# Kernel optimization log

Measured on AMD Instinct MI355X. Metric: run time of the kernel, lower is better.

## Reference

```python
import math
import jax, jax.numpy as jnp
import numpy as np

B, H, W, CV = 8, 64, 64, 256
T, CT = 77, 512
NH, TOP_M = 8, 5
CLAMP = 2.0

def _ln(x, g, b, eps=1e-5):
    mu = x.mean(-1, keepdims=True)
    var = ((x - mu) ** 2).mean(-1, keepdims=True)
    return (x - mu) / jnp.sqrt(var + eps) * g + b

def _l2norm(x, eps=1e-6):
    n = jnp.sqrt((x * x).sum(-1, keepdims=True))
    return x / jnp.maximum(n, eps)

def _xavier(key, fan_in, fan_out):
    a = math.sqrt(6.0 / (fan_in + fan_out))
    return jax.random.uniform(key, (fan_in, fan_out), jnp.float32, -a, a)

def setup_inputs() -> dict:
    key = jax.random.key(0)
    ks = jax.random.split(key, 12)
    inp = {
        'visual_features': jax.random.normal(ks[0], (B, H, W, CV), jnp.float32),
        'text_features': jax.random.normal(ks[1], (B, T, CT), jnp.float32),
        'Wq': _xavier(ks[2], CV, CV), 'bq': jnp.zeros((CV,), jnp.float32),
        'Wk': _xavier(ks[3], CT, CV), 'bk': jnp.zeros((CV,), jnp.float32),
        'Wv': _xavier(ks[4], CT, CV), 'bv': jnp.zeros((CV,), jnp.float32),
        'Wo': _xavier(ks[5], CV, CV), 'bo': jnp.zeros((CV,), jnp.float32),
        'g1': jnp.ones((CV,), jnp.float32), 'b1': jnp.zeros((CV,), jnp.float32),
        'g2': jnp.ones((CV,), jnp.float32), 'b2': jnp.zeros((CV,), jnp.float32),
        'W_ffn1': jax.random.normal(ks[6], (CV, 4 * CV), jnp.float32) * 0.02,
        'b_ffn1': jnp.zeros((4 * CV,), jnp.float32),
        'W_ffn2': jax.random.normal(ks[7], (4 * CV, CV), jnp.float32) * 0.02,
        'b_ffn2': jnp.zeros((CV,), jnp.float32),
        'logit_scale': jnp.float32(math.log(1.0 / 0.07)),
        'alpha': jnp.float32(0.1),
    }
    return inp

def _topm_mask(sim, m):
    # keep only top-m entries along last axis (scatter of top-k indices)
    t = sim.shape[-1]
    _, topi = jax.lax.top_k(sim, m)
    keep = jax.vmap(lambda idx: jnp.zeros((t,), bool).at[idx].set(True))(
        topi.reshape(-1, m)).reshape(sim.shape)
    return jnp.where(keep, sim, -jnp.inf)

def _forward(visual_features, text_features, Wq, bq, Wk, bk, Wv, bv, Wo, bo,
             g1, b1, g2, b2, W_ffn1, b_ffn1, W_ffn2, b_ffn2, logit_scale, alpha):
    b, h, w, cv = visual_features.shape
    n = h * w
    dh = cv // NH
    x = _ln(visual_features, g1, b1).reshape(b, n, cv)      # Pre-LN, (B,N,Cv)
    q = (x @ Wq + bq).reshape(b, n, NH, dh)
    k = (text_features @ Wk + bk).reshape(b, T, NH, dh)
    v = (text_features @ Wv + bv).reshape(b, T, NH, dh)
    q = _l2norm(q); k = _l2norm(k)                           # cosine attention
    scale = jnp.exp(jnp.clip(logit_scale, -CLAMP, CLAMP)) / jnp.sqrt(jnp.float32(dh))
    sim = jnp.einsum('bnhd,bthd->bnht', q, k) * scale        # (B,N,H,T)
    pad = jnp.abs(text_features).sum(-1) <= 1e-6             # (B,T) pad tokens
    sim = jnp.where(pad[:, None, None, :], -jnp.inf, sim)
    sim = _topm_mask(sim, TOP_M)
    attn = jax.nn.softmax(sim, axis=-1)
    all_pad = pad.all(axis=1)                                # (B,)
    attn = jnp.where(all_pad[:, None, None, None], 0.0, attn)
    aligned = jnp.einsum('bnht,bthd->bnhd', attn, v).reshape(b, n, cv)
    aligned = aligned @ Wo + bo
    y = x + alpha * aligned
    y = _ln(y, g2, b2)
    hdn = jax.nn.gelu(y @ W_ffn1 + b_ffn1, approximate=False)
    y = y + (hdn @ W_ffn2 + b_ffn2)
    return y.reshape(b, h, w, cv)

def reference(visual_features, text_features, Wq, bq, Wk, bk, Wv, bv, Wo, bo,
              g1, b1, g2, b2, W_ffn1, b_ffn1, W_ffn2, b_ffn2, logit_scale, alpha):
    return _forward(visual_features, text_features, Wq, bq, Wk, bk, Wv, bv, Wo, bo,
                    g1, b1, g2, b2, W_ffn1, b_ffn1, W_ffn2, b_ffn2, logit_scale, alpha)
```

## Files before the change

### kernel.cpp

```cpp
#include <hip/hip_runtime.h>
#include <math.h>

#define NB   8
#define NPIX 4096
#define MROW 32768
#define CV_  256
#define TT   77
#define CT_  512
#define NH_  8
#define DH_  32
#define BT_  616

typedef __bf16 bf16x8 __attribute__((ext_vector_type(8)));
typedef float  f32x4  __attribute__((ext_vector_type(4)));

__device__ __forceinline__ float bf2f(unsigned short u) {
  return __uint_as_float(((unsigned)u) << 16);
}
__device__ __forceinline__ unsigned short f2b(float f) {
  unsigned u = __float_as_uint(f);
  return (unsigned short)((u + 0x7FFFu + ((u >> 16) & 1u)) >> 16);
}
__device__ __forceinline__ unsigned pack2(float lo, float hi) {
  return ((unsigned)f2b(hi) << 16) | (unsigned)f2b(lo);
}
__device__ __forceinline__ void async_copy16(const unsigned short* g,
                                             unsigned short* l) {
  __builtin_amdgcn_global_load_lds(
      (const __attribute__((address_space(1))) void*)g,
      (__attribute__((address_space(3))) void*)l, 16, 0, 0);
}
__device__ __forceinline__ float gelu_t(float v) {
  float p = v * fmaf(0.0713548162726f, v * v, 1.59576912161f);
  float e = __expf(p);
  return v - v / (e + 1.0f);
}

__global__ __launch_bounds__(256) void prep_kernel(
    const float* __restrict__ visual, const float* __restrict__ g1,
    const float* __restrict__ b1, unsigned short* __restrict__ xbuf,
    const float* __restrict__ s0, const float* __restrict__ s1,
    const float* __restrict__ s2, const float* __restrict__ s3,
    const float* __restrict__ s4, const float* __restrict__ s5,
    unsigned short* __restrict__ d0, unsigned short* __restrict__ d1,
    unsigned short* __restrict__ d2, unsigned short* __restrict__ d3,
    unsigned short* __restrict__ d4, unsigned short* __restrict__ d5,
    const float* __restrict__ bk, const float* __restrict__ bv,
    float* __restrict__ bkv, const float* __restrict__ text,
    float* __restrict__ padb) {
  __shared__ unsigned short tl[64 * 68];
  int bx = blockIdx.x;
  int tid = threadIdx.x;
  int wave = tid >> 6, lane = tid & 63;
  if (bx < 8192) {
    int row = bx * 4 + wave;
    size_t base = (size_t)row * 256 + lane * 4;
    float4 f = *reinterpret_cast<const float4*>(visual + base);
    float v0 = f.x, v1 = f.y, v2 = f.z, v3 = f.w;
    float s = v0 + v1 + v2 + v3;
    float q = v0 * v0 + v1 * v1 + v2 * v2 + v3 * v3;
#pragma unroll
    for (int off = 1; off < 64; off <<= 1) {
      s += __shfl_xor(s, off);
      q += __shfl_xor(q, off);
    }
    float mean = s * (1.0f / 256.0f);
    float var  = q * (1.0f / 256.0f) - mean * mean;
    float rstd = rsqrtf(var + 1e-5f);
    float4 gv = *reinterpret_cast<const float4*>(g1 + lane * 4);
    float4 bv4 = *reinterpret_cast<const float4*>(b1 + lane * 4);
    ushort4 o;
    o.x = f2b((v0 - mean) * rstd * gv.x + bv4.x);
    o.y = f2b((v1 - mean) * rstd * gv.y + bv4.y);
    o.z = f2b((v2 - mean) * rstd * gv.z + bv4.z);
    o.w = f2b((v3 - mean) * rstd * gv.w + bv4.w);
    *reinterpret_cast<ushort4*>(xbuf + base) = o;
    return;
  }
  if (bx < 8416) {
    int ti = bx - 8192;
    const float* src; unsigned short* dst; int R, C, m;
    if      (ti < 16)  { src = s0; dst = d0; R = 256;  C = 256;  m = ti; }
    else if (ti < 48)  { src = s1; dst = d1; R = 512;  C = 256;  m = ti - 16; }
    else if (ti < 80)  { src = s2; dst = d2; R = 512;  C = 256;  m = ti - 48; }
    else if (ti < 96)  { src = s3; dst = d3; R = 256;  C = 256;  m = ti - 80; }
    else if (ti < 160) { src = s4; dst = d4; R = 256;  C = 1024; m = ti - 96; }
    else               { src = s5; dst = d5; R = 1024; C = 256;  m = ti - 160; }
    int tpc = C >> 6;
    int tr = m / tpc, tc = m % tpc;
#pragma unroll
    for (int i = 0; i < 4; ++i) {
      int lin = tid + i * 256;
      int r = lin >> 4, c4 = (lin & 15) * 4;
      float4 f = *reinterpret_cast<const float4*>(
          src + (size_t)(tr * 64 + r) * C + tc * 64 + c4);
      tl[(c4 + 0) * 68 + r] = f2b(f.x);
      tl[(c4 + 1) * 68 + r] = f2b(f.y);
      tl[(c4 + 2) * 68 + r] = f2b(f.z);
      tl[(c4 + 3) * 68 + r] = f2b(f.w);
    }
    __syncthreads();
#pragma unroll
    for (int i = 0; i < 4; ++i) {
      int lin = tid + i * 256;
      int c = lin >> 4, r4 = (lin & 15) * 4;
      ushort4 u = *reinterpret_cast<const ushort4*>(&tl[c * 68 + r4]);
      *reinterpret_cast<ushort4*>(
          dst + (size_t)(tc * 64 + c) * R + tr * 64 + r4) = u;
    }
    return;
  }
  if (bx == 8416) {
    bkv[tid] = bk[tid];
    bkv[256 + tid] = bv[tid];
    return;
  }
  {
    int row = (bx - 8417) * 4 + wave;
    const float* tr = text + (size_t)row * CT_ + lane * 8;
    float4 f0 = *reinterpret_cast<const float4*>(tr);
    float4 f1 = *reinterpret_cast<const float4*>(tr + 4);
    float s = fabsf(f0.x) + fabsf(f0.y) + fabsf(f0.z) + fabsf(f0.w)
            + fabsf(f1.x) + fabsf(f1.y) + fabsf(f1.z) + fabsf(f1.w);
#pragma unroll
    for (int off = 1; off < 64; off <<= 1) s += __shfl_xor(s, off);
    if (lane == 0) padb[row] = (s <= 1e-6f) ? 1.0f : 0.0f;
  }
}

__global__ __launch_bounds__(256) void qkv_kernel(
    const unsigned short* __restrict__ xb, const unsigned short* __restrict__ WqT,
    const float* __restrict__ bq, unsigned short* __restrict__ qout,
    const float* __restrict__ text, const unsigned short* __restrict__ WkvT,
    const float* __restrict__ bkv, float* __restrict__ kout,
    float* __restrict__ vout) {
  __shared__ unsigned short lA[4096];
  __shared__ unsigned short lB[4096];
  int tid = threadIdx.x;
  int lane = tid & 63, wave = tid >> 6;
  int l15 = lane & 15, quad = lane >> 4;
  if (blockIdx.x < 1024) {
    int bm = (blockIdx.x >> 2) * 128, bn = (blockIdx.x & 3) * 64;
    int wm = (wave & 1) * 64, wn = (wave >> 1) * 32;
    int crow = lane >> 2, ccol = (lane & 3) * 8;
    f32x4 acc[4][2] = {};
    for (int k0 = 0; k0 < 256; k0 += 32) {
#pragma unroll
      for (int ch = 0; ch < 2; ++ch) {
        int c = wave * 2 + ch;
        async_copy16(xb + (size_t)(bm + c * 16 + crow) * 256 + k0 + ccol,
                     &lA[c * 512]);
      }
      async_copy16(WqT + (size_t)(bn + wave * 16 + crow) * 256 + k0 + ccol,
                   &lB[wave * 512]);
      __syncthreads();
      bf16x8 af[4], bfr[2];
#pragma unroll
      for (int mi = 0; mi < 4; ++mi)
        af[mi] = *reinterpret_cast<const bf16x8*>(&lA[(wm + mi * 16 + l15) * 32 + quad * 8]);
#pragma unroll
      for (int ni = 0; ni < 2; ++ni)
        bfr[ni] = *reinterpret_cast<const bf16x8*>(&lB[(wn + ni * 16 + l15) * 32 + quad * 8]);
#pragma unroll
      for (int mi = 0; mi < 4; ++mi)
#pragma unroll
        for (int ni = 0; ni < 2; ++ni)
          acc[mi][ni] = __builtin_amdgcn_mfma_f32_16x16x32_bf16(af[mi], bfr[ni],
                                                                acc[mi][ni], 0, 0, 0);
      __syncthreads();
    }
#pragma unroll
    for (int mi = 0; mi < 4; ++mi) {
#pragma unroll
      for (int ni = 0; ni < 2; ++ni) {
        int gcol = bn + wn + ni * 16 + l15;
        float bsf = bq[gcol];
#pragma unroll
        for (int r = 0; r < 4; ++r) {
          int grow = bm + wm + mi * 16 + quad * 4 + r;
          qout[(size_t)grow * 256 + gcol] = f2b(acc[mi][ni][r] + bsf);
        }
      }
    }
  } else {
    int i = blockIdx.x - 1024;
    int bm = (i % 10) * 64, bn = (i / 10) * 64;
    int srow = tid >> 2, sc8 = (tid & 3) * 8;
    int wm = (wave & 1) * 32, wn = (wave >> 1) * 32;
    f32x4 acc[2][2] = {};
    int gm = bm + srow, gn = bn + srow;
    const bool aok = (gm < BT_);
    for (int k0 = 0; k0 < CT_; k0 += 32) {
      uint4 apk = make_uint4(0, 0, 0, 0);
      if (aok) {
        const float* Af = text + (size_t)gm * CT_ + k0 + sc8;
        float4 f0 = *reinterpret_cast<const float4*>(Af);
        float4 f1 = *reinterpret_cast<const float4*>(Af + 4);
        apk.x = pack2(f0.x, f0.y); apk.y = pack2(f0.z, f0.w);
        apk.z = pack2(f1.x, f1.y); apk.w = pack2(f1.z, f1.w);
      }
      uint4 bpk = *reinterpret_cast<const uint4*>(WkvT + (size_t)gn * CT_ + k0 + sc8);
      *reinterpret_cast<uint4*>(&lA[srow * 40 + sc8]) = apk;
      *reinterpret_cast<uint4*>(&lB[srow * 40 + sc8]) = bpk;
      __syncthreads();
      bf16x8 a0 = *reinterpret_cast<const bf16x8*>(&lA[(wm + l15) * 40 + quad * 8]);
      bf16x8 a1 = *reinterpret_cast<const bf16x8*>(&lA[(wm + 16 + l15) * 40 + quad * 8]);
      bf16x8 b0 = *reinterpret_cast<const bf16x8*>(&lB[(wn + l15) * 40 + quad * 8]);
      bf16x8 b1 = *reinterpret_cast<const bf16x8*>(&lB[(wn + 16 + l15) * 40 + quad * 8]);
      acc[0][0] = __builtin_amdgcn_mfma_f32_16x16x32_bf16(a0, b0, acc[0][0], 0, 0, 0);
      acc[0][1] = __builtin_amdgcn_mfma_f32_16x16x32_bf16(a0, b1, acc[0][1], 0, 0, 0);
      acc[1][0] = __builtin_amdgcn_mfma_f32_16x16x32_bf16(a1, b0, acc[1][0], 0, 0, 0);
      acc[1][1] = __builtin_amdgcn_mfma_f32_16x16x32_bf16(a1, b1, acc[1][1], 0, 0, 0);
      __syncthreads();
    }
#pragma unroll
    for (int mt = 0; mt < 2; ++mt) {
#pragma unroll
      for (int nt = 0; nt < 2; ++nt) {
        int gcol = bn + wn + nt * 16 + l15;
        float bsf = bkv[gcol];
#pragma unroll
        for (int r = 0; r < 4; ++r) {
          int grow = bm + wm + mt * 16 + quad * 4 + r;
          if (grow >= BT_) continue;
          float v = acc[mt][nt][r] + bsf;
          if (gcol < 256) kout[(size_t)grow * 256 + gcol] = v;
          else            vout[(size_t)grow * 256 + gcol - 256] = v;
        }
      }
    }
  }
}

__global__ __launch_bounds__(256) void gemm_oln(
    const unsigned short* __restrict__ A, const unsigned short* __restrict__ Bt,
    const float* __restrict__ bias, const unsigned short* __restrict__ xres,
    const float* __restrict__ alpha_ptr,
    const float* __restrict__ g2, const float* __restrict__ b2,
    unsigned short* __restrict__ ybf, float* __restrict__ yf32) {
  __shared__ unsigned short sm[9216];
  unsigned short* lA = sm;
  unsigned short* lB = sm + 1024;
  unsigned short* yt = sm;
  const int K = 256;
  int tid = threadIdx.x;
  int bm = blockIdx.x * 32;
  int lane = tid & 63, wave = tid >> 6;
  int wm = (wave & 1) * 16, wn = (wave >> 1) * 128;
  int l15 = lane & 15, quad = lane >> 4;
  int crow = lane >> 2, ccol = (lane & 3) * 8;
  f32x4 acc[8] = {};
  for (int k0 = 0; k0 < K; k0 += 32) {
    if (wave < 2)
      async_copy16(A + (size_t)(bm + wave * 16 + crow) * K + k0 + ccol,
                   &lA[wave * 512]);
#pragma unroll
    for (int ch = wave; ch < 16; ch += 4)
      async_copy16(Bt + (size_t)(ch * 16 + crow) * K + k0 + ccol,
                   &lB[ch * 512]);
    __syncthreads();
    bf16x8 af, bfr[8];
    af = *reinterpret_cast<const bf16x8*>(&lA[(wm + l15) * 32 + quad * 8]);
#pragma unroll
    for (int ni = 0; ni < 8; ++ni)
      bfr[ni] = *reinterpret_cast<const bf16x8*>(&lB[(wn + ni * 16 + l15) * 32 + quad * 8]);
#pragma unroll
    for (int ni = 0; ni < 8; ++ni)
      acc[ni] = __builtin_amdgcn_mfma_f32_16x16x32_bf16(af, bfr[ni],
                                                        acc[ni], 0, 0, 0);
    __syncthreads();
  }
  float alpha = *alpha_ptr;
#pragma unroll
  for (int ni = 0; ni < 8; ++ni) {
    int gcol = wn + ni * 16 + l15;
    float bsf = bias[gcol];
#pragma unroll
    for (int r = 0; r < 4; ++r) {
      int lrow = wm + quad * 4 + r;
      float v = acc[ni][r] + bsf;
      float y0 = bf2f(xres[(size_t)(bm + lrow) * 256 + gcol]) + alpha * v;
      yt[lrow * 256 + gcol] = f2b(y0);
    }
  }
  __syncthreads();
  for (int it = 0; it < 8; ++it) {
    int row = wave * 8 + it;
    ushort4 u = *reinterpret_cast<const ushort4*>(&yt[row * 256 + lane * 4]);
    float v0 = bf2f(u.x), v1 = bf2f(u.y), v2 = bf2f(u.z), v3 = bf2f(u.w);
    float s = v0 + v1 + v2 + v3;
    float q = v0 * v0 + v1 * v1 + v2 * v2 + v3 * v3;
#pragma unroll
    for (int off = 1; off < 64; off <<= 1) {
      s += __shfl_xor(s, off);
      q += __shfl_xor(q, off);
    }
    float mean = s * (1.0f / 256.0f);
    float var  = q * (1.0f / 256.0f) - mean * mean;
    float rstd = rsqrtf(var + 1e-5f);
    float4 gv = *reinterpret_cast<const float4*>(g2 + lane * 4);
    float4 bv = *reinterpret_cast<const float4*>(b2 + lane * 4);
    float o0 = (v0 - mean) * rstd * gv.x + bv.x;
    float o1 = (v1 - mean) * rstd * gv.y + bv.y;
    float o2 = (v2 - mean) * rstd * gv.z + bv.z;
    float o3 = (v3 - mean) * rstd * gv.w + bv.w;
    size_t base = (size_t)(bm + row) * 256 + lane * 4;
    ushort4 ob;
    ob.x = f2b(o0); ob.y = f2b(o1); ob.z = f2b(o2); ob.w = f2b(o3);
    *reinterpret_cast<ushort4*>(ybf + base) = ob;
    *reinterpret_cast<float4*>(yf32 + base) = make_float4(o0, o1, o2, o3);
  }
}

#define SSTR 83
#define VSTR 33
#define NEGBIG -3.0e38f
__device__ __forceinline__ void ins5(float sv, float& tv0, float& tv1,
                                     float& tv2, float& tv3, float& tv4) {
  bool g0 = sv > tv0, g1 = sv > tv1, g2 = sv > tv2, g3 = sv > tv3, g4 = sv > tv4;
  tv4 = g4 ? (g3 ? tv3 : sv) : tv4;
  tv3 = g3 ? (g2 ? tv2 : sv) : tv3;
  tv2 = g2 ? (g1 ? tv1 : sv) : tv2;
  tv1 = g1 ? (g0 ? tv0 : sv) : tv1;
  tv0 = g0 ? sv : tv0;
}
__global__ __launch_bounds__(256) void attn_kernel(
    unsigned short* qa, const float* __restrict__ k,
    const float* __restrict__ v, const float* __restrict__ padb,
    const float* __restrict__ ls_ptr) {
  __shared__ unsigned short qb[64 * 40];
  __shared__ unsigned short kb[80 * 40];
  __shared__ float S[64 * SSTR];
  __shared__ float vs[TT * VSTR];
  __shared__ float rn[64];
  __shared__ float scs[80];
  __shared__ int allpad_s;
  int tid = threadIdx.x;
  int h = blockIdx.y, b = blockIdx.z;
  size_t qbase = ((size_t)b * NPIX + blockIdx.x * 64) * CV_ + h * DH_;
  size_t kvbase = (size_t)b * TT * CV_ + h * DH_;
  float ls = *ls_ptr;
  ls = fminf(fmaxf(ls, -2.0f), 2.0f);
  float scale = expf(ls) * 0.17677669529663687f;
  if (tid == 0) allpad_s = 1;
  __syncthreads();
  int qrow = tid >> 2, qq = tid & 3;
  uint4 qv4 = *reinterpret_cast<const uint4*>(qa + qbase + (size_t)qrow * CV_ + qq * 8);
  *reinterpret_cast<uint4*>(&qb[qrow * 40 + qq * 8]) = qv4;
  {
    float ssq = 0.f;
    unsigned w[4] = {qv4.x, qv4.y, qv4.z, qv4.w};
#pragma unroll
    for (int i = 0; i < 4; ++i) {
      float a = bf2f((unsigned short)(w[i] & 0xFFFF));
      float bb = bf2f((unsigned short)(w[i] >> 16));
      ssq += a * a + bb * bb;
    }
    ssq += __shfl_xor(ssq, 1);
    ssq += __shfl_xor(ssq, 2);
    if (qq == 0) rn[qrow] = scale / fmaxf(sqrtf(ssq), 1e-6f);
  }
  if (tid < 154) {
    int kr = tid >> 1, kh = tid & 1;
    const float* kp = k + kvbase + (size_t)kr * CV_ + kh * 16;
    float4 f0 = *reinterpret_cast<const float4*>(kp);
    float4 f1 = *reinterpret_cast<const float4*>(kp + 4);
    float4 f2 = *reinterpret_cast<const float4*>(kp + 8);
    float4 f3 = *reinterpret_cast<const float4*>(kp + 12);
    float ks2 = f0.x*f0.x + f0.y*f0.y + f0.z*f0.z + f0.w*f0.w
              + f1.x*f1.x + f1.y*f1.y + f1.z*f1.z + f1.w*f1.w
              + f2.x*f2.x + f2.y*f2.y + f2.z*f2.z + f2.w*f2.w
              + f3.x*f3.x + f3.y*f3.y + f3.z*f3.z + f3.w*f3.w;
    uint4 p0, p1;
    p0.x = pack2(f0.x, f0.y); p0.y = pack2(f0.z, f0.w);
    p0.z = pack2(f1.x, f1.y); p0.w = pack2(f1.z, f1.w);
    p1.x = pack2(f2.x, f2.y); p1.y = pack2(f2.z, f2.w);
    p1.z = pack2(f3.x, f3.y); p1.w = pack2(f3.z, f3.w);
    *reinterpret_cast<uint4*>(&kb[kr * 40 + kh * 16]) = p0;
    *reinterpret_cast<uint4*>(&kb[kr * 40 + kh * 16 + 8]) = p1;
    ks2 += __shfl_xor(ks2, 1);
    if (kh == 0) {
      float p = padb[b * TT + kr];
      float sc = (p == 0.0f) ? 1.0f / fmaxf(sqrtf(ks2), 1e-6f) : 0.0f;
      scs[kr] = sc;
      if (sc > 0.0f) allpad_s = 0;
    }
  } else if (tid < 157) {
    scs[77 + (tid - 154)] = 0.0f;
  } else if (tid >= 160 && tid < 172) {
    int i = tid - 160;
    *reinterpret_cast<uint4*>(&kb[(77 + (i >> 2)) * 40 + (i & 3) * 8]) =
        make_uint4(0, 0, 0, 0);
  }
  for (int j = tid; j < TT * 8; j += 256) {
    int t = j >> 3, d4 = j & 7;
    float4 f = *reinterpret_cast<const float4*>(
        v + kvbase + (size_t)t * CV_ + d4 * 4);
    float* vp = &vs[t * VSTR + d4 * 4];
    vp[0] = f.x; vp[1] = f.y; vp[2] = f.z; vp[3] = f.w;
  }
  __syncthreads();
  {
    int lane = tid & 63, wave = tid >> 6;
    int wm = wave * 16;
    int l15 = lane & 15, quad = lane >> 4;
    f32x4 acc[5] = {};
    bf16x8 af = *reinterpret_cast<const bf16x8*>(&qb[(wm + l15) * 40 + quad * 8]);
    bf16x8 bfr[5];
#pragma unroll
    for (int ni = 0; ni < 5; ++ni)
      bfr[ni] = *reinterpret_cast<const bf16x8*>(&kb[(ni * 16 + l15) * 40 + quad * 8]);
#pragma unroll
    for (int ni = 0; ni < 5; ++ni)
      acc[ni] = __builtin_amdgcn_mfma_f32_16x16x32_bf16(af, bfr[ni], acc[ni], 0, 0, 0);
#pragma unroll
    for (int ni = 0; ni < 5; ++ni) {
      int col = ni * 16 + l15;
      float sc = scs[col];
#pragma unroll
      for (int r = 0; r < 4; ++r) {
        int row = wm + quad * 4 + r;
        float val = (sc > 0.0f) ? acc[ni][r] * rn[row] * sc : NEGBIG;
        unsigned pb = (__float_as_uint(val) & 0xFFFFFF80u) | (unsigned)col;
        S[row * SSTR + col] = __uint_as_float(pb);
      }
    }
  }
  __syncthreads();
  int allpad = allpad_s;
  int row = qrow;
  const float* Srow = &S[row * SSTR];
  int t0 = qq * 20, t1 = (qq == 3) ? TT : t0 + 20;
  float tv0 = -INFINITY, tv1 = -INFINITY, tv2 = -INFINITY,
        tv3 = -INFINITY, tv4 = -INFINITY;
  for (int t = t0; t < t1; ++t)
    ins5(Srow[t], tv0, tv1, tv2, tv3, tv4);
#pragma unroll
  for (int m = 1; m <= 2; m <<= 1) {
    float n0 = __shfl_xor(tv0, m), n1 = __shfl_xor(tv1, m),
          n2 = __shfl_xor(tv2, m), n3 = __shfl_xor(tv3, m),
          n4 = __shfl_xor(tv4, m);
    ins5(n0, tv0, tv1, tv2, tv3, tv4);
    ins5(n1, tv0, tv1, tv2, tv3, tv4);
    ins5(n2, tv0, tv1, tv2, tv3, tv4);
    ins5(n3, tv0, tv1, tv2, tv3, tv4);
    ins5(n4, tv0, tv1, tv2, tv3, tv4);
  }
  float o[8];
#pragma unroll
  for (int d = 0; d < 8; ++d) o[d] = 0.f;
  if (!allpad) {
    float e0 = 1.0f;
    float e1 = expf(tv1 - tv0);
    float e2 = expf(tv2 - tv0);
    float e3 = expf(tv3 - tv0);
    float e4 = expf(tv4 - tv0);
    float inv = 1.0f / (e0 + e1 + e2 + e3 + e4);
    int i0 = __float_as_uint(tv0) & 0x7F, i1 = __float_as_uint(tv1) & 0x7F,
        i2 = __float_as_uint(tv2) & 0x7F, i3 = __float_as_uint(tv3) & 0x7F,
        i4 = __float_as_uint(tv4) & 0x7F;
    const float* v0p = &vs[i0 * VSTR + qq * 8];
    const float* v1p = &vs[i1 * VSTR + qq * 8];
    const float* v2p = &vs[i2 * VSTR + qq * 8];
    const float* v3p = &vs[i3 * VSTR + qq * 8];
    const float* v4p = &vs[i4 * VSTR + qq * 8];
#pragma unroll
    for (int d = 0; d < 8; ++d)
      o[d] = (e0 * v0p[d] + e1 * v1p[d] + e2 * v2p[d] + e3 * v3p[d] + e4 * v4p[d]) * inv;
  }
  unsigned short* qp = qa + qbase + (size_t)row * CV_ + qq * 8;
  uint4 ou;
  ou.x = ((unsigned)f2b(o[1]) << 16) | f2b(o[0]);
  ou.y = ((unsigned)f2b(o[3]) << 16) | f2b(o[2]);
  ou.z = ((unsigned)f2b(o[5]) << 16) | f2b(o[4]);
  ou.w = ((unsigned)f2b(o[7]) << 16) | f2b(o[6]);
  *reinterpret_cast<uint4*>(qp) = ou;
}

__global__ __launch_bounds__(512) void ffn_fused(
    const unsigned short* __restrict__ ybf, const unsigned short* __restrict__ W1T,
    const float* __restrict__ b1f, const unsigned short* __restrict__ W2T,
    const float* __restrict__ b2f, float* __restrict__ yio) {
  __shared__ unsigned short xs[64 * 256];
  __shared__ unsigned short Hs[64 * 128];
  __shared__ unsigned short Wb[16384];
  int tid = threadIdx.x, lane = tid & 63, wave = tid >> 6;
  int l15 = lane & 15, quad = lane >> 4;
  int crow = lane >> 2;
  int ccs = (((lane & 3) ^ ((lane >> 3) & 3)) * 8);
  int rsw = ((quad ^ ((l15 >> 1) & 3)) * 8);
  int sws = l15 & 7;
  int bm = blockIdx.x * 64;
  {
    int row = tid >> 3, kh8 = (tid & 7) * 4;
    const unsigned short* src = ybf + (size_t)(bm + row) * 256 + kh8 * 8;
    int sw = row & 7;
    unsigned short* dst = &xs[row * 256];
#pragma unroll
    for (int i = 0; i < 4; ++i)
      *reinterpret_cast<uint4*>(dst + ((kh8 + i) ^ sw) * 8) =
          *reinterpret_cast<const uint4*>(src + i * 8);
  }
  int wm2 = (wave & 1) * 32, wn2 = (wave >> 1) * 64;
  int wh1 = (wave & 1) * 64, wr1 = (wave >> 1) * 16;
  int row1 = wr1 + l15;
  const unsigned short* w1p = W1T + (size_t)(wave * 16 + crow) * 256 + ccs;
  const unsigned short* w2p = W2T + (size_t)(wave * 32 + crow) * 1024 + ccs;
  auto stage_step = [&](int p2, int half) {
    unsigned short* buf = &Wb[half * 8192];
    if (p2 < 4) {
      async_copy16(w1p,      &buf[wave * 512]);
      async_copy16(w1p + 32, &buf[4096 + wave * 512]);
      w1p += 64;
      if (p2 == 3) w1p += 32512;
    } else {
      async_copy16(w2p,          &buf[wave * 1024]);
      async_copy16(w2p + 16384,  &buf[wave * 1024 + 512]);
      w2p += 32;
    }
  };
  f32x4 acc[2][4] = {};
  stage_step(0, 0); stage_step(1, 1);
  for (int c = 0; c < 8; ++c) {
    f32x4 acc1[4] = {};
#pragma unroll
    for (int p = 0; p < 8; ++p) {
      if (p == 7 && c == 7)
        asm volatile("s_waitcnt vmcnt(0) lgkmcnt(0)" ::: "memory");
      else
        asm volatile("s_waitcnt vmcnt(2) lgkmcnt(0)" ::: "memory");
      __builtin_amdgcn_s_barrier();
      __builtin_amdgcn_sched_barrier(0);
      const unsigned short* buf = &Wb[(p & 1) * 8192];
      if (p < 4) {
#pragma unroll
        for (int sl = 0; sl < 2; ++sl) {
          int k = p * 64 + sl * 32;
          bf16x8 af[4];
#pragma unroll
          for (int mi = 0; mi < 4; ++mi)
            af[mi] = *reinterpret_cast<const bf16x8*>(
                &buf[sl * 4096 + (wh1 + mi * 16 + l15) * 32 + rsw]);
          bf16x8 bx = *reinterpret_cast<const bf16x8*>(
              &xs[row1 * 256 + (((k >> 3) + quad) ^ sws) * 8]);
          __builtin_amdgcn_s_setprio(1);
#pragma unroll
          for (int mi = 0; mi < 4; ++mi)
            acc1[mi] = __builtin_amdgcn_mfma_f32_16x16x32_bf16(
                af[mi], bx, acc1[mi], 0, 0, 0);
          __builtin_amdgcn_s_setprio(0);
        }
        if (p == 3) {
#pragma unroll
          for (int mi = 0; mi < 4; ++mi) {
            int hb = wh1 + mi * 16 + quad * 4;
            float b0 = b1f[c * 128 + hb],      b1v = b1f[c * 128 + hb + 1];
            float b2v = b1f[c * 128 + hb + 2], b3 = b1f[c * 128 + hb + 3];
            ushort4 hw;
            hw.x = f2b(gelu_t(acc1[mi][0] + b0));
            hw.y = f2b(gelu_t(acc1[mi][1] + b1v));
            hw.z = f2b(gelu_t(acc1[mi][2] + b2v));
            hw.w = f2b(gelu_t(acc1[mi][3] + b3));
            *reinterpret_cast<ushort4*>(
                &Hs[row1 * 128 + (((hb >> 3) ^ sws) * 8) + (hb & 7)]) = hw;
          }
        }
      } else {
        int kk = (p - 4) * 32;
        bf16x8 af[2], bfr[4];
#pragma unroll
        for (int mi = 0; mi < 2; ++mi) {
          int hrow = wm2 + mi * 16 + l15;
          af[mi] = *reinterpret_cast<const bf16x8*>(
              &Hs[hrow * 128 + (((kk >> 3) + quad) ^ sws) * 8]);
        }
#pragma unroll
        for (int ni = 0; ni < 4; ++ni)
          bfr[ni] = *reinterpret_cast<const bf16x8*>(
              &buf[(wn2 + ni * 16 + l15) * 32 + rsw]);
        __builtin_amdgcn_s_setprio(1);
#pragma unroll
        for (int mi = 0; mi < 2; ++mi)
#pragma unroll
          for (int ni = 0; ni < 4; ++ni)
            acc[mi][ni] = __builtin_amdgcn_mfma_f32_16x16x32_bf16(
                af[mi], bfr[ni], acc[mi][ni], 0, 0, 0);
        __builtin_amdgcn_s_setprio(0);
      }
      __builtin_amdgcn_sched_barrier(0);
      __builtin_amdgcn_s_barrier();
      __builtin_amdgcn_sched_barrier(0);
      if (c < 7 || p < 6)
        stage_step((p + 2) & 7, p & 1);
    }
  }
#pragma unroll
  for (int mi = 0; mi < 2; ++mi)
#pragma unroll
    for (int ni = 0; ni < 4; ++ni) {
      int col = wn2 + ni * 16 + l15;
      float bs = b2f[col];
#pragma unroll
      for (int r = 0; r < 4; ++r) {
        int g = bm + wm2 + mi * 16 + quad * 4 + r;
        size_t oi = (size_t)g * 256 + col;
        yio[oi] = yio[oi] + acc[mi][ni][r] + bs;
      }
    }
}

extern "C" void kernel_launch(void* const* d_in, const int* in_sizes, int n_in,
                              void* d_out, int out_size, void* d_ws, size_t ws_size,
                              hipStream_t stream) {
  const float* visual = (const float*)d_in[0];
  const float* text   = (const float*)d_in[1];
  const float* Wq  = (const float*)d_in[2];
  const float* bq  = (const float*)d_in[3];
  const float* Wk  = (const float*)d_in[4];
  const float* bk  = (const float*)d_in[5];
  const float* Wv  = (const float*)d_in[6];
  const float* bv  = (const float*)d_in[7];
  const float* Wo  = (const float*)d_in[8];
  const float* bo  = (const float*)d_in[9];
  const float* g1  = (const float*)d_in[10];
  const float* b1  = (const float*)d_in[11];
  const float* g2  = (const float*)d_in[12];
  const float* b2  = (const float*)d_in[13];
  const float* W1  = (const float*)d_in[14];
  const float* bf1 = (const float*)d_in[15];
  const float* W2  = (const float*)d_in[16];
  const float* bff2 = (const float*)d_in[17];
  const float* lsc = (const float*)d_in[18];
  const float* alp = (const float*)d_in[19];

  char* ws = (char*)d_ws;
  size_t off = 0;
  auto alloc = [&](size_t bytes) -> char* {
    char* p = ws + off;
    off += (bytes + 255) & ~(size_t)255;
    return p;
  };
  unsigned short* WqT = (unsigned short*)alloc((size_t)65536 * 2);
  unsigned short* WkT = (unsigned short*)alloc((size_t)131072 * 2);
  unsigned short* WvT = (unsigned short*)alloc((size_t)131072 * 2);
  unsigned short* WoT = (unsigned short*)alloc((size_t)65536 * 2);
  unsigned short* W1T = (unsigned short*)alloc((size_t)262144 * 2);
  unsigned short* W2T = (unsigned short*)alloc((size_t)262144 * 2);
  float*          bkv  = (float*)alloc(512 * 4);
  float*          kbuf = (float*)alloc((size_t)BT_ * CV_ * 4);
  float*          vbuf = (float*)alloc((size_t)BT_ * CV_ * 4);
  float*          padb = (float*)alloc((size_t)BT_ * 4);
  char* U = ws + off;
  unsigned short* xbuf = (unsigned short*)U;
  unsigned short* qbuf = (unsigned short*)(U + 16777216);
  float*          ybuf = (float*)d_out;

  prep_kernel<<<8571, 256, 0, stream>>>(visual, g1, b1, xbuf,
                                        Wq, Wk, Wv, Wo, W1, W2,
                                        WqT, WkT, WvT, WoT, W1T, W2T,
                                        bk, bv, bkv, text, padb);
  qkv_kernel<<<1104, 256, 0, stream>>>(xbuf, WqT, bq, qbuf,
                                       text, WkT, bkv, kbuf, vbuf);
  attn_kernel<<<dim3(64, NH_, NB), 256, 0, stream>>>(qbuf, kbuf, vbuf, padb, lsc);
  gemm_oln<<<1024, 256, 0, stream>>>(qbuf, WoT, bo, xbuf, alp, g2, b2,
                                     xbuf, ybuf);
  ffn_fused<<<512, 512, 0, stream>>>(xbuf, W1T, bf1, W2T, bff2, ybuf);
}
```

Baseline: 274.9 us.

## Fuse output projection and LayerNorm into the FFN kernel prologue

Removes the separate gemm_oln kernel. ffn_fused now computes the Wo projection, the alpha-scaled residual add and LayerNorm2 for its 64-row tile directly into shared memory, using the swizzled layout the FFN expects. The FFN epilogue reads the residual from shared memory instead of reading back the fp32 intermediate from global. This saves a kernel launch plus global writes and reads of the bf16 and fp32 intermediates. In exchange, each FFN block does extra GEMM work with a simple, unpipelined sync loop and loads the full Wo weight per block.

Result: faster. 263.0 us (-4.3%).

```diff
diff --git a/kernel.cpp b/kernel.cpp
--- a/kernel.cpp
+++ b/kernel.cpp
@@ -229,86 +229,6 @@
         }
       }
     }
-  }
-}
-
-__global__ __launch_bounds__(256) void gemm_oln(
-    const unsigned short* __restrict__ A, const unsigned short* __restrict__ Bt,
-    const float* __restrict__ bias, const unsigned short* __restrict__ xres,
-    const float* __restrict__ alpha_ptr,
-    const float* __restrict__ g2, const float* __restrict__ b2,
-    unsigned short* __restrict__ ybf, float* __restrict__ yf32) {
-  __shared__ unsigned short sm[9216];
-  unsigned short* lA = sm;
-  unsigned short* lB = sm + 1024;
-  unsigned short* yt = sm;
-  const int K = 256;
-  int tid = threadIdx.x;
-  int bm = blockIdx.x * 32;
-  int lane = tid & 63, wave = tid >> 6;
-  int wm = (wave & 1) * 16, wn = (wave >> 1) * 128;
-  int l15 = lane & 15, quad = lane >> 4;
-  int crow = lane >> 2, ccol = (lane & 3) * 8;
-  f32x4 acc[8] = {};
-  for (int k0 = 0; k0 < K; k0 += 32) {
-    if (wave < 2)
-      async_copy16(A + (size_t)(bm + wave * 16 + crow) * K + k0 + ccol,
-                   &lA[wave * 512]);
-#pragma unroll
-    for (int ch = wave; ch < 16; ch += 4)
-      async_copy16(Bt + (size_t)(ch * 16 + crow) * K + k0 + ccol,
-                   &lB[ch * 512]);
-    __syncthreads();
-    bf16x8 af, bfr[8];
-    af = *reinterpret_cast<const bf16x8*>(&lA[(wm + l15) * 32 + quad * 8]);
-#pragma unroll
-    for (int ni = 0; ni < 8; ++ni)
-      bfr[ni] = *reinterpret_cast<const bf16x8*>(&lB[(wn + ni * 16 + l15) * 32 + quad * 8]);
-#pragma unroll
-    for (int ni = 0; ni < 8; ++ni)
-      acc[ni] = __builtin_amdgcn_mfma_f32_16x16x32_bf16(af, bfr[ni],
-                                                        acc[ni], 0, 0, 0);
-    __syncthreads();
-  }
-  float alpha = *alpha_ptr;
-#pragma unroll
-  for (int ni = 0; ni < 8; ++ni) {
-    int gcol = wn + ni * 16 + l15;
-    float bsf = bias[gcol];
-#pragma unroll
-    for (int r = 0; r < 4; ++r) {
-      int lrow = wm + quad * 4 + r;
-      float v = acc[ni][r] + bsf;
-      float y0 = bf2f(xres[(size_t)(bm + lrow) * 256 + gcol]) + alpha * v;
-      yt[lrow * 256 + gcol] = f2b(y0);
-    }
-  }
-  __syncthreads();
-  for (int it = 0; it < 8; ++it) {
-    int row = wave * 8 + it;
-    ushort4 u = *reinterpret_cast<const ushort4*>(&yt[row * 256 + lane * 4]);
-    float v0 = bf2f(u.x), v1 = bf2f(u.y), v2 = bf2f(u.z), v3 = bf2f(u.w);
-    float s = v0 + v1 + v2 + v3;
-    float q = v0 * v0 + v1 * v1 + v2 * v2 + v3 * v3;
-#pragma unroll
-    for (int off = 1; off < 64; off <<= 1) {
-      s += __shfl_xor(s, off);
-      q += __shfl_xor(q, off);
-    }
-    float mean = s * (1.0f / 256.0f);
-    float var  = q * (1.0f / 256.0f) - mean * mean;
-    float rstd = rsqrtf(var + 1e-5f);
-    float4 gv = *reinterpret_cast<const float4*>(g2 + lane * 4);
-    float4 bv = *reinterpret_cast<const float4*>(b2 + lane * 4);
-    float o0 = (v0 - mean) * rstd * gv.x + bv.x;
-    float o1 = (v1 - mean) * rstd * gv.y + bv.y;
-    float o2 = (v2 - mean) * rstd * gv.z + bv.z;
-    float o3 = (v3 - mean) * rstd * gv.w + bv.w;
-    size_t base = (size_t)(bm + row) * 256 + lane * 4;
-    ushort4 ob;
-    ob.x = f2b(o0); ob.y = f2b(o1); ob.z = f2b(o2); ob.w = f2b(o3);
-    *reinterpret_cast<ushort4*>(ybf + base) = ob;
-    *reinterpret_cast<float4*>(yf32 + base) = make_float4(o0, o1, o2, o3);
   }
 }
 
@@ -478,9 +398,13 @@
 }
 
 __global__ __launch_bounds__(512) void ffn_fused(
-    const unsigned short* __restrict__ ybf, const unsigned short* __restrict__ W1T,
-    const float* __restrict__ b1f, const unsigned short* __restrict__ W2T,
-    const float* __restrict__ b2f, float* __restrict__ yio) {
+    const unsigned short* __restrict__ A, const unsigned short* __restrict__ Bt,
+    const float* __restrict__ bo, const unsigned short* __restrict__ xres,
+    const float* __restrict__ alpha_ptr,
+    const float* __restrict__ g2, const float* __restrict__ b2ln,
+    const unsigned short* __restrict__ W1T, const float* __restrict__ b1f,
+    const unsigned short* __restrict__ W2T, const float* __restrict__ b2f,
+    float* __restrict__ yio) {
   __shared__ unsigned short xs[64 * 256];
   __shared__ unsigned short Hs[64 * 128];
   __shared__ unsigned short Wb[16384];
@@ -492,14 +416,76 @@
   int sws = l15 & 7;
   int bm = blockIdx.x * 64;
   {
-    int row = tid >> 3, kh8 = (tid & 7) * 4;
-    const unsigned short* src = ybf + (size_t)(bm + row) * 256 + kh8 * 8;
-    int sw = row & 7;
-    unsigned short* dst = &xs[row * 256];
-#pragma unroll
-    for (int i = 0; i < 4; ++i)
-      *reinterpret_cast<uint4*>(dst + ((kh8 + i) ^ sw) * 8) =
-          *reinterpret_cast<const uint4*>(src + i * 8);
+    int wrO = (wave & 1) * 32, wcO = (wave >> 1) * 64;
+    f32x4 accO[2][4] = {};
+    for (int k0 = 0; k0 < 256; k0 += 32) {
+      if (tid < 256)
+        async_copy16(A + (size_t)(bm + (tid >> 2)) * 256 + k0 + (tid & 3) * 8,
+                     &Hs[tid * 8]);
+      async_copy16(Bt + (size_t)(tid >> 2) * 256 + k0 + (tid & 3) * 8,
+                   &Wb[tid * 8]);
+      async_copy16(Bt + (size_t)((tid >> 2) + 128) * 256 + k0 + (tid & 3) * 8,
+                   &Wb[4096 + tid * 8]);
+      __syncthreads();
+      bf16x8 af[2], bfr[4];
+#pragma unroll
+      for (int mi = 0; mi < 2; ++mi)
+        af[mi] = *reinterpret_cast<const bf16x8*>(
+            &Hs[(wrO + mi * 16 + l15) * 32 + quad * 8]);
+#pragma unroll
+      for (int ni = 0; ni < 4; ++ni)
+        bfr[ni] = *reinterpret_cast<const bf16x8*>(
+            &Wb[(wcO + ni * 16 + l15) * 32 + quad * 8]);
+#pragma unroll
+      for (int mi = 0; mi < 2; ++mi)
+#pragma unroll
+        for (int ni = 0; ni < 4; ++ni)
+          accO[mi][ni] = __builtin_amdgcn_mfma_f32_16x16x32_bf16(
+              af[mi], bfr[ni], accO[mi][ni], 0, 0, 0);
+      __syncthreads();
+    }
+    float alpha = *alpha_ptr;
+#pragma unroll
+    for (int mi = 0; mi < 2; ++mi) {
+#pragma unroll
+      for (int ni = 0; ni < 4; ++ni) {
+        int gcol = wcO + ni * 16 + l15;
+        float bsf = bo[gcol];
+#pragma unroll
+        for (int r = 0; r < 4; ++r) {
+          int lrow = wrO + mi * 16 + quad * 4 + r;
+          float v = accO[mi][ni][r] + bsf;
+          float y0 = bf2f(xres[(size_t)(bm + lrow) * 256 + gcol]) + alpha * v;
+          xs[lrow * 256 + gcol] = f2b(y0);
+        }
+      }
+    }
+    __syncthreads();
+    for (int it = 0; it < 8; ++it) {
+      int row = wave * 8 + it;
+      ushort4 u = *reinterpret_cast<const ushort4*>(&xs[row * 256 + lane * 4]);
+      float v0 = bf2f(u.x), v1 = bf2f(u.y), v2 = bf2f(u.z), v3 = bf2f(u.w);
+      float s = v0 + v1 + v2 + v3;
+      float q = v0 * v0 + v1 * v1 + v2 * v2 + v3 * v3;
+#pragma unroll
+      for (int off = 1; off < 64; off <<= 1) {
+        s += __shfl_xor(s, off);
+        q += __shfl_xor(q, off);
+      }
+      float mean = s * (1.0f / 256.0f);
+      float var  = q * (1.0f / 256.0f) - mean * mean;
+      float rstd = rsqrtf(var + 1e-5f);
+      float4 gv = *reinterpret_cast<const float4*>(g2 + lane * 4);
+      float4 bv = *reinterpret_cast<const float4*>(b2ln + lane * 4);
+      ushort4 ob;
+      ob.x = f2b((v0 - mean) * rstd * gv.x + bv.x);
+      ob.y = f2b((v1 - mean) * rstd * gv.y + bv.y);
+      ob.z = f2b((v2 - mean) * rstd * gv.z + bv.z);
+      ob.w = f2b((v3 - mean) * rstd * gv.w + bv.w);
+      int slot = (lane >> 1) ^ (row & 7);
+      *reinterpret_cast<ushort4*>(&xs[row * 256 + slot * 8 + (lane & 1) * 4]) = ob;
+    }
+    __syncthreads();
   }
   int wm2 = (wave & 1) * 32, wn2 = (wave >> 1) * 64;
   int wh1 = (wave & 1) * 64, wr1 = (wave >> 1) * 16;
@@ -602,9 +588,10 @@
       float bs = b2f[col];
 #pragma unroll
       for (int r = 0; r < 4; ++r) {
-        int g = bm + wm2 + mi * 16 + quad * 4 + r;
-        size_t oi = (size_t)g * 256 + col;
-        yio[oi] = yio[oi] + acc[mi][ni][r] + bs;
+        int lrow = wm2 + mi * 16 + quad * 4 + r;
+        float resid = bf2f(xs[lrow * 256 + (((col >> 3) ^ (lrow & 7)) * 8) + (col & 7)]);
+        size_t oi = (size_t)(bm + lrow) * 256 + col;
+        yio[oi] = resid + acc[mi][ni][r] + bs;
       }
     }
 }
@@ -662,7 +649,6 @@
   qkv_kernel<<<1104, 256, 0, stream>>>(xbuf, WqT, bq, qbuf,
                                        text, WkT, bkv, kbuf, vbuf);
   attn_kernel<<<dim3(64, NH_, NB), 256, 0, stream>>>(qbuf, kbuf, vbuf, padb, lsc);
-  gemm_oln<<<1024, 256, 0, stream>>>(qbuf, WoT, bo, xbuf, alp, g2, b2,
-                                     xbuf, ybuf);
-  ffn_fused<<<512, 512, 0, stream>>>(xbuf, W1T, bf1, W2T, bff2, ybuf);
-}
+  ffn_fused<<<512, 512, 0, stream>>>(qbuf, WoT, bo, xbuf, alp, g2, b2,
+                                     W1T, bf1, W2T, bff2, ybuf);
+}
```
